# Kernel tuning notes

Measured on AMD Instinct MI355X. Metric: run time of the kernel, lower is better.

The kernel has to match this reference:

```python
import jax, jax.numpy as jnp
import numpy as np

V, E, H, W, S, T, B = 10000, 256, 512, 256, 512, 128, 64


def setup_inputs() -> dict:
    key = jax.random.key(0)
    ks = jax.random.split(key, 17)
    def rn(k, shape, s=0.08):
        return jax.random.normal(k, shape, jnp.float32) * s
    return {
        "tokens": jax.random.randint(ks[0], (B, S), 0, V),
        "dec_h0": jax.random.normal(ks[1], (B, H), jnp.float32),
        "emb_table": rn(ks[2], (V, E), 1.0),
        "enc_Wih": rn(ks[3], (4 * H, E)),
        "enc_Whh": rn(ks[4], (4 * H, H)),
        "enc_bih": rn(ks[5], (4 * H,)),
        "enc_bhh": rn(ks[6], (4 * H,)),
        "dec_Wih": rn(ks[7], (4 * H, E)),
        "dec_Whh": rn(ks[8], (4 * H, H)),
        "dec_bih": rn(ks[9], (4 * H,)),
        "dec_bhh": rn(ks[10], (4 * H,)),
        "W1_w": rn(ks[11], (W, H)),
        "W1_b": rn(ks[12], (W,)),
        "W2_w": rn(ks[13], (W, H)),
        "W2_b": rn(ks[14], (W,)),
        "vt_w": rn(ks[15], (1, W)),
        "vt_b": rn(ks[16], (1,)),
    }


def _lstm_cell(x, h, c, Wih, Whh, bih, bhh):
    # PyTorch gate order: input, forget, cell(g), output
    gates = x @ Wih.T + h @ Whh.T + bih + bhh
    i, f, g, o = jnp.split(gates, 4, axis=-1)
    c = jax.nn.sigmoid(f) * c + jax.nn.sigmoid(i) * jnp.tanh(g)
    h = jax.nn.sigmoid(o) * jnp.tanh(c)
    return h, c


def reference(tokens, dec_h0, emb_table, enc_Wih, enc_Whh, enc_bih, enc_bhh,
              dec_Wih, dec_Whh, dec_bih, dec_bhh, W1_w, W1_b, W2_w, W2_b,
              vt_w, vt_b):
    emb = emb_table[tokens]                       # [B,S,E]
    x_sbe = jnp.swapaxes(emb, 0, 1)               # [S,B,E] time-major
    bsz = tokens.shape[0]
    h0 = jnp.zeros((bsz, enc_Whh.shape[1]), emb.dtype)

    def enc_step(carry, x):
        h, c = carry
        h, c = _lstm_cell(x, h, c, enc_Wih, enc_Whh, enc_bih, enc_bhh)
        return (h, c), h

    _, enc_states = jax.lax.scan(enc_step, (h0, h0), x_sbe)   # [S,B,H]

    # W1(encoder_states) is constant across decoder steps -> hoist it
    blend1 = enc_states @ W1_w.T + W1_b            # [S,B,W]
    c0 = enc_states[-1]                            # original uses last enc state as cell init
    dec_in = jnp.zeros((bsz, emb_table.shape[1]), emb.dtype)  # never updated in original

    def dec_step(carry, _):
        h, c = carry
        h, c = _lstm_cell(dec_in, h, c, dec_Wih, dec_Whh, dec_bih, dec_bhh)
        blend2 = h @ W2_w.T + W2_b                 # [B,W]
        u = (jnp.tanh(blend1 + blend2[None]) @ vt_w.T)[..., 0] + vt_b[0]  # [S,B]
        logp = jax.nn.log_softmax(u.T, axis=1)     # [B,S], softmax over seq positions
        return (h, c), logp

    _, probs = jax.lax.scan(dec_step, (dec_h0, c0), None, length=T)  # [T,B,S]
    return jnp.swapaxes(probs, 0, 1)               # [B,T,S]
```

## Files before the change

### kernel.cpp

```cpp
#include <hip/hip_runtime.h>
#include <hip/hip_bf16.h>
#include <cstdint>
#include <cstddef>

typedef __bf16 bf16_t;
typedef __bf16 bf16x8 __attribute__((ext_vector_type(8)));
typedef float  f32x4  __attribute__((ext_vector_type(4)));

#define NB 64
#define NS 512
#define NTD 128
#define NE 256
#define NH 512
#define NG 2048
#define NW 256

#define HSTEP_DW 16384u

__device__ __forceinline__ float sigm_f(float x) { return 1.f / (1.f + __expf(-x)); }
__device__ __forceinline__ float tanh_f(float x) {
  float e = __expf(2.f * x);
  return 1.f - 2.f / (e + 1.f);
}
__device__ __forceinline__ float bits2f(uint32_t b16) {
  uint32_t u = b16 << 16;
  return __builtin_bit_cast(float, u);
}
__device__ __forceinline__ uint32_t packh(float a, float b) {
  uint16_t lo = __builtin_bit_cast(uint16_t, (bf16_t)a);
  uint16_t hi = __builtin_bit_cast(uint16_t, (bf16_t)b);
  return (uint32_t)lo | ((uint32_t)hi << 16);
}
__device__ __forceinline__ uint32_t aload(const uint32_t* p) {
  return __hip_atomic_load(p, __ATOMIC_RELAXED, __HIP_MEMORY_SCOPE_AGENT);
}
__device__ __forceinline__ uint64_t aload64(const uint64_t* p) {
  return __hip_atomic_load(p, __ATOMIC_RELAXED, __HIP_MEMORY_SCOPE_AGENT);
}
__device__ __forceinline__ void astore(uint32_t* p, uint32_t v) {
  __hip_atomic_store(p, v, __ATOMIC_RELAXED, __HIP_MEMORY_SCOPE_AGENT);
}
__device__ __forceinline__ void astoref(float* p, float v) {
  __hip_atomic_store((uint32_t*)p, __builtin_bit_cast(uint32_t, v),
                     __ATOMIC_RELAXED, __HIP_MEMORY_SCOPE_AGENT);
}
__device__ __forceinline__ float aloadf(const float* p) {
  return __builtin_bit_cast(float, aload((const uint32_t*)p));
}

__global__ __launch_bounds__(256) void pack_b(const float* __restrict__ src,
                                              bf16_t* __restrict__ dst,
                                              int N, int K) {
  int idx = blockIdx.x * 256 + threadIdx.x;
  if (idx >= N * K) return;
  int n = idx / K, k = idx - n * K;
  int lane = (((k & 31) >> 3) << 4) | (n & 15);
  size_t o = ((((size_t)(n >> 4) * (K >> 5)) + (k >> 5)) * 64 + lane) * 8 + (k & 7);
  dst[o] = (bf16_t)src[idx];
}

__global__ __launch_bounds__(256) void gather_emb(const int* __restrict__ tokens,
                                                  const float* __restrict__ table,
                                                  bf16_t* __restrict__ embfrag) {
  int idx = blockIdx.x * 256 + threadIdx.x;
  int row = idx >> 5, e0 = (idx & 31) << 3;
  int b = row & 63, s = row >> 6;
  int tok = tokens[b * NS + s];
  const float4* p = (const float4*)(table + (size_t)tok * NE + e0);
  float4 v0 = p[0], v1 = p[1];
  bf16x8 v;
  v[0] = (bf16_t)v0.x; v[1] = (bf16_t)v0.y; v[2] = (bf16_t)v0.z; v[3] = (bf16_t)v0.w;
  v[4] = (bf16_t)v1.x; v[5] = (bf16_t)v1.y; v[6] = (bf16_t)v1.z; v[7] = (bf16_t)v1.w;
  int mt = row >> 4;
  int ks = e0 >> 5;
  int lane = (b & 15) | (((e0 >> 3) & 3) << 4);
  *(bf16x8*)(embfrag + ((size_t)(mt * 8 + ks) * 64 + lane) * 8) = v;
}

__global__ __launch_bounds__(256) void pack_h0(const float* __restrict__ src,
                                               uint32_t* __restrict__ dst) {
  int idx = blockIdx.x * 256 + threadIdx.x;
  int b = idx >> 8, jp = idx & 255;
  int j = jp * 2;
  float lo = src[(size_t)b * NH + j], hi = src[(size_t)b * NH + j + 1];
  int bg = b >> 4, bl = b & 15, ks = j >> 5;
  int lane = bl | (((j >> 3) & 3) << 4);
  dst[((size_t)bg * 16 + ks) * 256 + lane * 4 + ((j >> 1) & 3)] = packh(lo, hi);
}

template <typename OutT, int KS, int MT>
__global__ __launch_bounds__(256) void gemm_fa2(const bf16_t* __restrict__ A,
                                                const bf16_t* __restrict__ Bp,
                                                OutT* __restrict__ out,
                                                const float* __restrict__ bias1,
                                                const float* __restrict__ bias2,
                                                int N) {
  int lane = threadIdx.x & 63, w = threadIdx.x >> 6;
  int nt = blockIdx.x * 4 + w;
  int mt0 = blockIdx.y * MT;
  bf16x8 bfr[KS];
  const bf16_t* bp = Bp + ((size_t)nt * KS * 64 + lane) * 8;
#pragma unroll
  for (int ks = 0; ks < KS; ++ks) bfr[ks] = *(const bf16x8*)(bp + (size_t)ks * 512);
  int col = (nt << 4) + (lane & 15);
  float bs = bias1[col] + (bias2 ? bias2[col] : 0.f);
  for (int m = 0; m < MT; ++m) {
    int mt = mt0 + m;
    const bf16_t* ap = A + (size_t)mt * (KS * 512) + lane * 8;
    f32x4 acc = {0.f, 0.f, 0.f, 0.f};
#pragma unroll
    for (int ks = 0; ks < KS; ++ks)
      acc = __builtin_amdgcn_mfma_f32_16x16x32_bf16(
          *(const bf16x8*)(ap + (size_t)ks * 512), bfr[ks], acc, 0, 0, 0);
    int rbase = (mt << 4) + ((lane >> 4) << 2);
#pragma unroll
    for (int r = 0; r < 4; ++r)
      out[(size_t)(rbase + r) * N + col] = (OutT)(acc[r] + bs);
  }
}

__global__ __launch_bounds__(256) void enc_chain(
    const bf16_t* __restrict__ Wp, const bf16_t* __restrict__ xih,
    const bf16_t* __restrict__ W1p, const float* __restrict__ W1_b,
    uint32_t* __restrict__ hfrag, uint32_t* __restrict__ flags,
    bf16_t* __restrict__ blend1) {
  __shared__ bf16_t wlds[8 * 8192];
  __shared__ bf16_t w1lds[8192];
  __shared__ float gl[4][16][36];
  const int T = NS;
  int tid = threadIdx.x, lane = tid & 63, wv = tid >> 6;
  int bg = blockIdx.x >> 4, slice = blockIdx.x & 15;

  for (int l = 0; l < 8; ++l) {
    int g = l >> 1, p = l & 1;
    const bf16_t* src = Wp + (size_t)(g * 32 + slice * 2 + p) * 8192;
    bf16_t* dst = wlds + (size_t)l * 8192;
    for (int i = tid; i < 1024; i += 256)
      *(bf16x8*)(dst + (size_t)i * 8) = *(const bf16x8*)(src + (size_t)i * 8);
  }
  {
    const bf16_t* src = W1p + (size_t)slice * 8192;
    for (int i = tid; i < 1024; i += 256)
      *(bf16x8*)(w1lds + (size_t)i * 8) = *(const bf16x8*)(src + (size_t)i * 8);
  }

  int ub = tid >> 4, uj2 = tid & 15;
  int lane_f = ub | ((uj2 >> 2) << 4);
  float c0 = 0.f, c1 = 0.f;
  float b1bias = W1_b[slice * 16 + (lane & 15)];
  __syncthreads();

  const uint64_t* hq = (const uint64_t*)hfrag;
  uint32_t* fl = flags + bg * 16;

  for (int t = 0; t <= T; ++t) {
    uint32_t xd[4];
    if (t < T) {
      const uint32_t* xr = (const uint32_t*)xih +
          ((size_t)(t * 64 + bg * 16 + ub)) * 1024 + slice * 16 + uj2;
#pragma unroll
      for (int g = 0; g < 4; ++g) xd[g] = xr[(size_t)g * 256];
    }
    if (t > 0) {
      if (wv == 0) {
        uint32_t tgt = (uint32_t)t;
        bool ok;
        do {
          uint32_t f = tgt;
          if (lane < 16 && lane != (uint32_t)slice) f = aload(fl + lane);
          ok = __all(f >= tgt);
        } while (!ok);
      }
      __syncthreads();
    }
    const uint64_t* hb = hq + ((size_t)t * 4 + bg) * 2048 + lane * 2;
    uint64_t aq[16][2];
#pragma unroll
    for (int ks = 0; ks < 16; ++ks) {
      aq[ks][0] = aload64(hb + (size_t)ks * 128);
      aq[ks][1] = aload64(hb + (size_t)ks * 128 + 1);
    }
    if (t >= 1 && wv == 0) {
      f32x4 bacc = {0.f, 0.f, 0.f, 0.f};
#pragma unroll
      for (int ks = 0; ks < 16; ++ks) {
        union { uint64_t q[2]; bf16x8 v; } u;
        u.q[0] = aq[ks][0]; u.q[1] = aq[ks][1];
        bacc = __builtin_amdgcn_mfma_f32_16x16x32_bf16(
            u.v, *(const bf16x8*)(w1lds + (size_t)ks * 512 + lane * 8), bacc, 0, 0, 0);
      }
      int col = slice * 16 + (lane & 15);
      int rb = (lane >> 4) << 2;
      size_t rowb = (size_t)(t - 1) * 64 + bg * 16 + rb;
#pragma unroll
      for (int r = 0; r < 4; ++r)
        blend1[(rowb + r) * 256 + col] = (bf16_t)(bacc[r] + b1bias);
    }
    if (t < T) {
      const bf16_t* wl = wlds + (size_t)(wv * 2) * 8192 + lane * 8;
      f32x4 acc0 = {0.f, 0.f, 0.f, 0.f}, acc1 = {0.f, 0.f, 0.f, 0.f};
#pragma unroll
      for (int ks = 0; ks < 16; ++ks) {
        union { uint64_t q[2]; bf16x8 v; } u;
        u.q[0] = aq[ks][0]; u.q[1] = aq[ks][1];
        acc0 = __builtin_amdgcn_mfma_f32_16x16x32_bf16(
            u.v, *(const bf16x8*)(wl + (size_t)ks * 512), acc0, 0, 0, 0);
        acc1 = __builtin_amdgcn_mfma_f32_16x16x32_bf16(
            u.v, *(const bf16x8*)(wl + 8192 + (size_t)ks * 512), acc1, 0, 0, 0);
      }
      int cc = lane & 15, rb = (lane >> 4) << 2;
#pragma unroll
      for (int r = 0; r < 4; ++r) {
        gl[wv][rb + r][cc] = acc0[r];
        gl[wv][rb + r][16 + cc] = acc1[r];
      }
      __syncthreads();
      float p[4][2];
#pragma unroll
      for (int g = 0; g < 4; ++g) {
        p[g][0] = gl[g][ub][uj2 * 2] + bits2f(xd[g] & 0xffffu);
        p[g][1] = gl[g][ub][uj2 * 2 + 1] + bits2f(xd[g] >> 16);
      }
      float i0 = sigm_f(p[0][0]), f0 = sigm_f(p[1][0]);
      float g0 = tanh_f(p[2][0]), o0 = sigm_f(p[3][0]);
      c0 = f0 * c0 + i0 * g0;
      float h0 = o0 * tanh_f(c0);
      float i1 = sigm_f(p[0][1]), f1 = sigm_f(p[1][1]);
      float g1 = tanh_f(p[2][1]), o1 = sigm_f(p[3][1]);
      c1 = f1 * c1 + i1 * g1;
      float h1 = o1 * tanh_f(c1);
      astore(hfrag + ((size_t)(t + 1) * 4 + bg) * 4096 +
                 slice * 256 + lane_f * 4 + (uj2 & 3), packh(h0, h1));
      __syncthreads();
      if (tid == 0) astore(fl + slice, (uint32_t)(t + 1));
    }
  }
}

__global__ __launch_bounds__(256) void dec_attn(
    const bf16_t* __restrict__ Wp, const float* __restrict__ bih,
    const float* __restrict__ bhh, const bf16_t* __restrict__ W2p,
    const float* __restrict__ W2_b, uint32_t* __restrict__ hfrag,
    const uint32_t* __restrict__ c0frag, uint32_t* __restrict__ hflags,
    uint32_t* __restrict__ bl2f, const bf16_t* __restrict__ blend1,
    float* __restrict__ blend2, const float* __restrict__ vt_w,
    float* __restrict__ out) {
  union SM {
    struct { bf16_t wlds[8 * 8192]; bf16_t w2lds[8192]; float gl[4][16][36]; } c;
    struct { float vt[272], b2[272], u[512], red[8]; } a;
  };
  __shared__ SM sm;
  const int T = NTD;
  int tid = threadIdx.x, lane = tid & 63, wv = tid >> 6;

  if (blockIdx.x < 64) {
    int bg = blockIdx.x >> 4, slice = blockIdx.x & 15;
    for (int l = 0; l < 8; ++l) {
      int g = l >> 1, p = l & 1;
      const bf16_t* src = Wp + (size_t)(g * 32 + slice * 2 + p) * 8192;
      bf16_t* dst = sm.c.wlds + (size_t)l * 8192;
      for (int i = tid; i < 1024; i += 256)
        *(bf16x8*)(dst + (size_t)i * 8) = *(const bf16x8*)(src + (size_t)i * 8);
    }
    {
      const bf16_t* src = W2p + (size_t)slice * 8192;
      for (int i = tid; i < 1024; i += 256)
        *(bf16x8*)(sm.c.w2lds + (size_t)i * 8) = *(const bf16x8*)(src + (size_t)i * 8);
    }
    int ub = tid >> 4, uj2 = tid & 15;
    int j_lo = slice * 32 + uj2 * 2;
    int lane_f = ub | ((uj2 >> 2) << 4);
    uint32_t d = c0frag[((size_t)bg * 16 + slice) * 256 + lane_f * 4 + (uj2 & 3)];
    float c0 = bits2f(d & 0xffffu), c1 = bits2f(d >> 16);
    float bsum[4][2];
#pragma unroll
    for (int g = 0; g < 4; ++g) {
      bsum[g][0] = bih[g * NH + j_lo] + bhh[g * NH + j_lo];
      bsum[g][1] = bih[g * NH + j_lo + 1] + bhh[g * NH + j_lo + 1];
    }
    float b2bias = W2_b[slice * 16 + (lane & 15)];
    __syncthreads();

    const uint64_t* hq = (const uint64_t*)hfrag;
    uint32_t* fl = hflags + bg * 16;

    for (int t = 0; t <= T; ++t) {
      if (t > 0) {
        if (wv == 0) {
          uint32_t tgt = (uint32_t)t;
          bool ok;
          do {
            uint32_t f = tgt;
            if (lane < 16 && lane != (uint32_t)slice) f = aload(fl + lane);
            ok = __all(f >= tgt);
          } while (!ok);
        }
        __syncthreads();
      }
      const uint64_t* hb = hq + ((size_t)t * 4 + bg) * 2048 + lane * 2;
      uint64_t aq[16][2];
#pragma unroll
      for (int ks = 0; ks < 16; ++ks) {
        aq[ks][0] = aload64(hb + (size_t)ks * 128);
        aq[ks][1] = aload64(hb + (size_t)ks * 128 + 1);
      }
      if (t >= 1 && wv == 0) {
        f32x4 bacc = {0.f, 0.f, 0.f, 0.f};
#pragma unroll
        for (int ks = 0; ks < 16; ++ks) {
          union { uint64_t q[2]; bf16x8 v; } u;
          u.q[0] = aq[ks][0]; u.q[1] = aq[ks][1];
          bacc = __builtin_amdgcn_mfma_f32_16x16x32_bf16(
              u.v, *(const bf16x8*)(sm.c.w2lds + (size_t)ks * 512 + lane * 8),
              bacc, 0, 0, 0);
        }
        int col = slice * 16 + (lane & 15);
        int rb = (lane >> 4) << 2;
        size_t rowb = (size_t)(t - 1) * 64 + bg * 16 + rb;
#pragma unroll
        for (int r = 0; r < 4; ++r)
          astoref(blend2 + (rowb + r) * 256 + col, bacc[r] + b2bias);
      }
      if (t < T) {
        const bf16_t* wl = sm.c.wlds + (size_t)(wv * 2) * 8192 + lane * 8;
        f32x4 acc0 = {0.f, 0.f, 0.f, 0.f}, acc1 = {0.f, 0.f, 0.f, 0.f};
#pragma unroll
        for (int ks = 0; ks < 16; ++ks) {
          union { uint64_t q[2]; bf16x8 v; } u;
          u.q[0] = aq[ks][0]; u.q[1] = aq[ks][1];
          acc0 = __builtin_amdgcn_mfma_f32_16x16x32_bf16(
              u.v, *(const bf16x8*)(wl + (size_t)ks * 512), acc0, 0, 0, 0);
          acc1 = __builtin_amdgcn_mfma_f32_16x16x32_bf16(
              u.v, *(const bf16x8*)(wl + 8192 + (size_t)ks * 512), acc1, 0, 0, 0);
        }
        int cc = lane & 15, rb = (lane >> 4) << 2;
#pragma unroll
        for (int r = 0; r < 4; ++r) {
          sm.c.gl[wv][rb + r][cc] = acc0[r];
          sm.c.gl[wv][rb + r][16 + cc] = acc1[r];
        }
        __syncthreads();
        float p[4][2];
#pragma unroll
        for (int g = 0; g < 4; ++g) {
          p[g][0] = sm.c.gl[g][ub][uj2 * 2] + bsum[g][0];
          p[g][1] = sm.c.gl[g][ub][uj2 * 2 + 1] + bsum[g][1];
        }
        float i0 = sigm_f(p[0][0]), f0 = sigm_f(p[1][0]);
        float g0 = tanh_f(p[2][0]), o0 = sigm_f(p[3][0]);
        c0 = f0 * c0 + i0 * g0;
        float h0 = o0 * tanh_f(c0);
        float i1 = sigm_f(p[0][1]), f1 = sigm_f(p[1][1]);
        float g1 = tanh_f(p[2][1]), o1 = sigm_f(p[3][1]);
        c1 = f1 * c1 + i1 * g1;
        float h1 = o1 * tanh_f(c1);
        astore(hfrag + ((size_t)(t + 1) * 4 + bg) * 4096 +
                   slice * 256 + lane_f * 4 + (uj2 & 3), packh(h0, h1));
        __syncthreads();
        if (tid == 0) {
          astore(fl + slice, (uint32_t)(t + 1));
          astore(bl2f + bg * 16 + slice, (uint32_t)t);
        }
      } else {
        __syncthreads();
        if (tid == 0) astore(bl2f + bg * 16 + slice, (uint32_t)T);
      }
    }
  } else {
    int w = blockIdx.x - 64;
    for (int k = w; k < NTD * NB; k += 192) {
      int t = k >> 6, b = k & 63;
      if (wv == 0) {
        uint32_t tgt = (uint32_t)(t + 1);
        bool ok;
        do {
          uint32_t f = aload(bl2f + lane);
          ok = __all(f >= tgt);
          if (!ok) __builtin_amdgcn_s_sleep(16);
        } while (!ok);
      }
      __syncthreads();
      {
        int ww = tid;
        int pi = ww + ((ww >> 6) << 2);
        sm.a.vt[pi] = vt_w[ww];
        sm.a.b2[pi] = aloadf(blend2 + (size_t)(t * 64 + b) * NW + ww);
      }
      __syncthreads();
      int wgrp = lane >> 4, sgrp = lane & 15;
      int base = wgrp * 68;
      for (int it = 0; it < 8; ++it) {
        int s = it * 64 + wv * 16 + sgrp;
        const bf16_t* row = blend1 + ((size_t)s * NB + b) * NW + wgrp * 64;
        float val = 0.f;
#pragma unroll
        for (int c8 = 0; c8 < 8; ++c8) {
          bf16x8 v = *(const bf16x8*)(row + c8 * 8);
#pragma unroll
          for (int jx = 0; jx < 8; ++jx) {
            int wi = base + c8 * 8 + jx;
            val += sm.a.vt[wi] * tanh_f((float)v[jx] + sm.a.b2[wi]);
          }
        }
        val += __shfl_xor(val, 16, 64);
        val += __shfl_xor(val, 32, 64);
        if (wgrp == 0) sm.a.u[it * 64 + wv * 16 + sgrp] = val;
      }
      __syncthreads();
      float a = sm.a.u[tid], bb2 = sm.a.u[tid + 256];
      float m = fmaxf(a, bb2);
#pragma unroll
      for (int o = 1; o < 64; o <<= 1) m = fmaxf(m, __shfl_xor(m, o, 64));
      if (lane == 0) sm.a.red[wv] = m;
      __syncthreads();
      m = fmaxf(fmaxf(sm.a.red[0], sm.a.red[1]), fmaxf(sm.a.red[2], sm.a.red[3]));
      float e = __expf(a - m) + __expf(bb2 - m);
#pragma unroll
      for (int o = 1; o < 64; o <<= 1) e += __shfl_xor(e, o, 64);
      if (lane == 0) sm.a.red[4 + wv] = e;
      __syncthreads();
      float lz = m + logf(sm.a.red[4] + sm.a.red[5] + sm.a.red[6] + sm.a.red[7]);
      size_t ob = ((size_t)b * NTD + t) * NS;
      out[ob + tid] = a - lz;
      out[ob + tid + 256] = bb2 - lz;
      __syncthreads();
    }
  }
}

extern "C" void kernel_launch(void* const* d_in, const int* in_sizes, int n_in,
                              void* d_out, int out_size, void* d_ws, size_t ws_size,
                              hipStream_t stream) {
  const int*   tokens    = (const int*)d_in[0];
  const float* dec_h0    = (const float*)d_in[1];
  const float* emb_table = (const float*)d_in[2];
  const float* enc_Wih   = (const float*)d_in[3];
  const float* enc_Whh   = (const float*)d_in[4];
  const float* enc_bih   = (const float*)d_in[5];
  const float* enc_bhh   = (const float*)d_in[6];
  const float* dec_Whh   = (const float*)d_in[8];
  const float* dec_bih   = (const float*)d_in[9];
  const float* dec_bhh   = (const float*)d_in[10];
  const float* W1_w      = (const float*)d_in[11];
  const float* W1_b      = (const float*)d_in[12];
  const float* W2_w      = (const float*)d_in[13];
  const float* W2_b      = (const float*)d_in[14];
  const float* vt_w      = (const float*)d_in[15];
  float* out = (float*)d_out;

  char* w = (char*)d_ws;
  size_t off = 0;
  auto alloc = [&](size_t bytes) {
    size_t o = off;
    off += (bytes + 255) & ~(size_t)255;
    return o;
  };
  bf16_t* embfrag = (bf16_t*)(w + alloc((size_t)NS * NB * NE * 2));
  bf16_t* xih     = (bf16_t*)(w + alloc((size_t)NS * NB * NG * 2));
  uint32_t* enc_hf = (uint32_t*)(w + alloc((size_t)(NS + 1) * HSTEP_DW * 4));
  uint32_t* dec_hf = (uint32_t*)(w + alloc((size_t)(NTD + 1) * HSTEP_DW * 4));
  bf16_t* blend1  = (bf16_t*)(w + alloc((size_t)NS * NB * NW * 2));
  float*  blend2  = (float*)(w + alloc((size_t)NTD * NB * NW * 4));
  bf16_t* pWih    = (bf16_t*)(w + alloc((size_t)NG * NE * 2));
  bf16_t* pWhhE   = (bf16_t*)(w + alloc((size_t)NG * NH * 2));
  bf16_t* pWhhD   = (bf16_t*)(w + alloc((size_t)NG * NH * 2));
  bf16_t* pW1     = (bf16_t*)(w + alloc((size_t)NW * NH * 2));
  bf16_t* pW2     = (bf16_t*)(w + alloc((size_t)NW * NH * 2));
  uint32_t* flags = (uint32_t*)(w + alloc(1024));
  (void)ws_size; (void)in_sizes; (void)n_in; (void)out_size;

  hipMemsetAsync(flags, 0, 768, stream);
  hipMemsetAsync(enc_hf, 0, HSTEP_DW * 4, stream);

  pack_b<<<(NG * NE) / 256, 256, 0, stream>>>(enc_Wih, pWih, NG, NE);
  pack_b<<<(NG * NH) / 256, 256, 0, stream>>>(enc_Whh, pWhhE, NG, NH);
  pack_b<<<(NG * NH) / 256, 256, 0, stream>>>(dec_Whh, pWhhD, NG, NH);
  pack_b<<<(NW * NH) / 256, 256, 0, stream>>>(W1_w, pW1, NW, NH);
  pack_b<<<(NW * NH) / 256, 256, 0, stream>>>(W2_w, pW2, NW, NH);

  gather_emb<<<(NS * NB * (NE / 8)) / 256, 256, 0, stream>>>(tokens, emb_table, embfrag);
  pack_h0<<<64, 256, 0, stream>>>(dec_h0, dec_hf);

  gemm_fa2<bf16_t, 8, 16><<<dim3(128 / 4, 2048 / 16), 256, 0, stream>>>(
      embfrag, pWih, xih, enc_bih, enc_bhh, NG);

  enc_chain<<<64, 256, 0, stream>>>(pWhhE, xih, pW1, W1_b, enc_hf, flags, blend1);

  dec_attn<<<256, 256, 0, stream>>>(pWhhD, dec_bih, dec_bhh, pW2, W2_b, dec_hf,
                                    enc_hf + (size_t)NS * HSTEP_DW, flags + 64,
                                    flags + 128, blend1, blend2, vt_w, out);
}
```

Measured before the change: 3.243 ms.

## Restructure LSTM recurrence waves to drop block barriers and use per-wave flags

The recurrent encoder and decoder blocks are reorganized so each of two waves computes all four gates for a 16-column tile directly in registers. This removes the LDS gate exchange and the block-wide __syncthreads in every timestep. A third wave independently computes the W1/W2 projection by polling per-wave padded flags, and the fourth wave exits. The input-projection GEMM now writes xih in a fragment layout matched to the new per-wave gate ownership. The cost is more flags to poll (32 per group) and an explicit vmcnt drain before each flag publish.

```diff
diff --git a/kernel.cpp b/kernel.cpp
--- a/kernel.cpp
+++ b/kernel.cpp
@@ -16,6 +16,7 @@
 #define NW 256
 
 #define HSTEP_DW 16384u
+#define FPAD 16
 
 __device__ __forceinline__ float sigm_f(float x) { return 1.f / (1.f + __expf(-x)); }
 __device__ __forceinline__ float tanh_f(float x) {
@@ -26,11 +27,6 @@
   uint32_t u = b16 << 16;
   return __builtin_bit_cast(float, u);
 }
-__device__ __forceinline__ uint32_t packh(float a, float b) {
-  uint16_t lo = __builtin_bit_cast(uint16_t, (bf16_t)a);
-  uint16_t hi = __builtin_bit_cast(uint16_t, (bf16_t)b);
-  return (uint32_t)lo | ((uint32_t)hi << 16);
-}
 __device__ __forceinline__ uint32_t aload(const uint32_t* p) {
   return __hip_atomic_load(p, __ATOMIC_RELAXED, __HIP_MEMORY_SCOPE_AGENT);
 }
@@ -46,6 +42,13 @@
 }
 __device__ __forceinline__ float aloadf(const float* p) {
   return __builtin_bit_cast(float, aload((const uint32_t*)p));
+}
+__device__ __forceinline__ void drain_vm() {
+  asm volatile("s_waitcnt vmcnt(0)" ::: "memory");
+}
+__device__ __forceinline__ float xpick(uint2 v, int r) {
+  uint32_t d = (r < 2) ? v.x : v.y;
+  return bits2f((r & 1) ? (d >> 16) : (d & 0xffffu));
 }
 
 __global__ __launch_bounds__(256) void pack_b(const float* __restrict__ src,
@@ -83,18 +86,20 @@
   int b = idx >> 8, jp = idx & 255;
   int j = jp * 2;
   float lo = src[(size_t)b * NH + j], hi = src[(size_t)b * NH + j + 1];
+  uint16_t l16 = __builtin_bit_cast(uint16_t, (bf16_t)lo);
+  uint16_t h16 = __builtin_bit_cast(uint16_t, (bf16_t)hi);
   int bg = b >> 4, bl = b & 15, ks = j >> 5;
   int lane = bl | (((j >> 3) & 3) << 4);
-  dst[((size_t)bg * 16 + ks) * 256 + lane * 4 + ((j >> 1) & 3)] = packh(lo, hi);
-}
-
-template <typename OutT, int KS, int MT>
-__global__ __launch_bounds__(256) void gemm_fa2(const bf16_t* __restrict__ A,
+  dst[((size_t)bg * 16 + ks) * 256 + lane * 4 + ((j >> 1) & 3)] =
+      (uint32_t)l16 | ((uint32_t)h16 << 16);
+}
+
+__global__ __launch_bounds__(256) void gemm_xih(const bf16_t* __restrict__ A,
                                                 const bf16_t* __restrict__ Bp,
-                                                OutT* __restrict__ out,
-                                                const float* __restrict__ bias1,
-                                                const float* __restrict__ bias2,
-                                                int N) {
+                                                bf16_t* __restrict__ out,
+                                                const float* __restrict__ b1,
+                                                const float* __restrict__ b2) {
+  const int KS = 8, MT = 16;
   int lane = threadIdx.x & 63, w = threadIdx.x >> 6;
   int nt = blockIdx.x * 4 + w;
   int mt0 = blockIdx.y * MT;
@@ -102,8 +107,9 @@
   const bf16_t* bp = Bp + ((size_t)nt * KS * 64 + lane) * 8;
 #pragma unroll
   for (int ks = 0; ks < KS; ++ks) bfr[ks] = *(const bf16x8*)(bp + (size_t)ks * 512);
-  int col = (nt << 4) + (lane & 15);
-  float bs = bias1[col] + (bias2 ? bias2[col] : 0.f);
+  int n = (nt << 4) + (lane & 15);
+  float bs = b1[n] + b2[n];
+  int g = nt >> 5, sl = (nt & 31) >> 1, ct = nt & 1;
   for (int m = 0; m < MT; ++m) {
     int mt = mt0 + m;
     const bf16_t* ap = A + (size_t)mt * (KS * 512) + lane * 8;
@@ -112,127 +118,127 @@
     for (int ks = 0; ks < KS; ++ks)
       acc = __builtin_amdgcn_mfma_f32_16x16x32_bf16(
           *(const bf16x8*)(ap + (size_t)ks * 512), bfr[ks], acc, 0, 0, 0);
-    int rbase = (mt << 4) + ((lane >> 4) << 2);
-#pragma unroll
-    for (int r = 0; r < 4; ++r)
-      out[(size_t)(rbase + r) * N + col] = (OutT)(acc[r] + bs);
+    ushort4 hv;
+    hv.x = __builtin_bit_cast(uint16_t, (bf16_t)(acc[0] + bs));
+    hv.y = __builtin_bit_cast(uint16_t, (bf16_t)(acc[1] + bs));
+    hv.z = __builtin_bit_cast(uint16_t, (bf16_t)(acc[2] + bs));
+    hv.w = __builtin_bit_cast(uint16_t, (bf16_t)(acc[3] + bs));
+    *(ushort4*)(out + ((((size_t)mt * 16 + sl) * 2 + ct) * 4 + g) * 256 + lane * 4) = hv;
   }
 }
 
 __global__ __launch_bounds__(256) void enc_chain(
-    const bf16_t* __restrict__ Wp, const bf16_t* __restrict__ xih,
+    const bf16_t* __restrict__ Wp, const bf16_t* __restrict__ xih2,
     const bf16_t* __restrict__ W1p, const float* __restrict__ W1_b,
     uint32_t* __restrict__ hfrag, uint32_t* __restrict__ flags,
     bf16_t* __restrict__ blend1) {
   __shared__ bf16_t wlds[8 * 8192];
-  __shared__ bf16_t w1lds[8192];
-  __shared__ float gl[4][16][36];
-  const int T = NS;
-  int tid = threadIdx.x, lane = tid & 63, wv = tid >> 6;
+  __shared__ bf16_t wb[8192];
+  int tid = threadIdx.x, lane = tid & 63, wid = tid >> 6;
   int bg = blockIdx.x >> 4, slice = blockIdx.x & 15;
 
   for (int l = 0; l < 8; ++l) {
     int g = l >> 1, p = l & 1;
-    const bf16_t* src = Wp + (size_t)(g * 32 + slice * 2 + p) * 8192;
-    bf16_t* dst = wlds + (size_t)l * 8192;
+    const bf16_t* s = Wp + (size_t)(g * 32 + slice * 2 + p) * 8192;
     for (int i = tid; i < 1024; i += 256)
-      *(bf16x8*)(dst + (size_t)i * 8) = *(const bf16x8*)(src + (size_t)i * 8);
+      *(bf16x8*)(wlds + l * 8192 + (size_t)i * 8) = *(const bf16x8*)(s + (size_t)i * 8);
   }
   {
-    const bf16_t* src = W1p + (size_t)slice * 8192;
+    const bf16_t* s = W1p + (size_t)slice * 8192;
     for (int i = tid; i < 1024; i += 256)
-      *(bf16x8*)(w1lds + (size_t)i * 8) = *(const bf16x8*)(src + (size_t)i * 8);
+      *(bf16x8*)(wb + (size_t)i * 8) = *(const bf16x8*)(s + (size_t)i * 8);
   }
-
-  int ub = tid >> 4, uj2 = tid & 15;
-  int lane_f = ub | ((uj2 >> 2) << 4);
-  float c0 = 0.f, c1 = 0.f;
-  float b1bias = W1_b[slice * 16 + (lane & 15)];
   __syncthreads();
+  if (wid == 3) return;
 
   const uint64_t* hq = (const uint64_t*)hfrag;
-  uint32_t* fl = flags + bg * 16;
-
-  for (int t = 0; t <= T; ++t) {
-    uint32_t xd[4];
-    if (t < T) {
-      const uint32_t* xr = (const uint32_t*)xih +
-          ((size_t)(t * 64 + bg * 16 + ub)) * 1024 + slice * 16 + uj2;
-#pragma unroll
-      for (int g = 0; g < 4; ++g) xd[g] = xr[(size_t)g * 256];
-    }
-    if (t > 0) {
-      if (wv == 0) {
-        uint32_t tgt = (uint32_t)t;
-        bool ok;
+  uint32_t* fbase = flags + bg * 32 * FPAD;
+  int c = lane & 15, grp = lane >> 4;
+
+  if (wid < 2) {
+    int ct = wid;
+    int j = slice * 32 + ct * 16 + c;
+    int sub = (j >> 3) & 3, dw = (j >> 1) & 3;
+    uint32_t* myflag = fbase + (slice * 2 + ct) * FPAD;
+    float cst[4] = {0.f, 0.f, 0.f, 0.f};
+    const bf16_t* wb0 = wlds + (size_t)(0 * 2 + ct) * 8192;
+    const bf16_t* wb1 = wlds + (size_t)(1 * 2 + ct) * 8192;
+    const bf16_t* wb2 = wlds + (size_t)(2 * 2 + ct) * 8192;
+    const bf16_t* wb3 = wlds + (size_t)(3 * 2 + ct) * 8192;
+    for (int t = 0; t < NS; ++t) {
+      const uint32_t* xb = (const uint32_t*)xih2 +
+          ((((size_t)t * 4 + bg) * 16 + slice) * 2 + ct) * 512 + lane * 2;
+      uint2 xg0 = *(const uint2*)(xb);
+      uint2 xg1 = *(const uint2*)(xb + 128);
+      uint2 xg2 = *(const uint2*)(xb + 256);
+      uint2 xg3 = *(const uint2*)(xb + 384);
+      if (t > 0) {
+        uint32_t tgt = (uint32_t)t; bool ok;
         do {
           uint32_t f = tgt;
-          if (lane < 16 && lane != (uint32_t)slice) f = aload(fl + lane);
+          if (lane < 32) f = aload(fbase + lane * FPAD);
           ok = __all(f >= tgt);
         } while (!ok);
       }
-      __syncthreads();
-    }
-    const uint64_t* hb = hq + ((size_t)t * 4 + bg) * 2048 + lane * 2;
-    uint64_t aq[16][2];
-#pragma unroll
-    for (int ks = 0; ks < 16; ++ks) {
-      aq[ks][0] = aload64(hb + (size_t)ks * 128);
-      aq[ks][1] = aload64(hb + (size_t)ks * 128 + 1);
-    }
-    if (t >= 1 && wv == 0) {
-      f32x4 bacc = {0.f, 0.f, 0.f, 0.f};
+      const uint64_t* hb = hq + ((size_t)t * 4 + bg) * 2048 + lane * 2;
+      uint64_t aq[16][2];
+#pragma unroll
+      for (int ks = 0; ks < 16; ++ks) {
+        aq[ks][0] = aload64(hb + (size_t)ks * 128);
+        aq[ks][1] = aload64(hb + (size_t)ks * 128 + 1);
+      }
+      f32x4 a0 = {0.f,0.f,0.f,0.f}, a1 = a0, a2 = a0, a3 = a0;
 #pragma unroll
       for (int ks = 0; ks < 16; ++ks) {
         union { uint64_t q[2]; bf16x8 v; } u;
         u.q[0] = aq[ks][0]; u.q[1] = aq[ks][1];
-        bacc = __builtin_amdgcn_mfma_f32_16x16x32_bf16(
-            u.v, *(const bf16x8*)(w1lds + (size_t)ks * 512 + lane * 8), bacc, 0, 0, 0);
-      }
-      int col = slice * 16 + (lane & 15);
-      int rb = (lane >> 4) << 2;
-      size_t rowb = (size_t)(t - 1) * 64 + bg * 16 + rb;
-#pragma unroll
-      for (int r = 0; r < 4; ++r)
-        blend1[(rowb + r) * 256 + col] = (bf16_t)(bacc[r] + b1bias);
-    }
-    if (t < T) {
-      const bf16_t* wl = wlds + (size_t)(wv * 2) * 8192 + lane * 8;
-      f32x4 acc0 = {0.f, 0.f, 0.f, 0.f}, acc1 = {0.f, 0.f, 0.f, 0.f};
+        int o = ks * 512 + lane * 8;
+        a0 = __builtin_amdgcn_mfma_f32_16x16x32_bf16(u.v, *(const bf16x8*)(wb0 + o), a0, 0, 0, 0);
+        a1 = __builtin_amdgcn_mfma_f32_16x16x32_bf16(u.v, *(const bf16x8*)(wb1 + o), a1, 0, 0, 0);
+        a2 = __builtin_amdgcn_mfma_f32_16x16x32_bf16(u.v, *(const bf16x8*)(wb2 + o), a2, 0, 0, 0);
+        a3 = __builtin_amdgcn_mfma_f32_16x16x32_bf16(u.v, *(const bf16x8*)(wb3 + o), a3, 0, 0, 0);
+      }
+      uint32_t hsb = ((uint32_t)(t + 1) * 4 + (uint32_t)bg) * 4096 + slice * 256;
+#pragma unroll
+      for (int r = 0; r < 4; ++r) {
+        float pi = a0[r] + xpick(xg0, r), pf = a1[r] + xpick(xg1, r);
+        float pg = a2[r] + xpick(xg2, r), po = a3[r] + xpick(xg3, r);
+        float iG = sigm_f(pi), fG = sigm_f(pf), gG = tanh_f(pg), oG = sigm_f(po);
+        cst[r] = fG * cst[r] + iG * gG;
+        float h = oG * tanh_f(cst[r]);
+        uint16_t hv = __builtin_bit_cast(uint16_t, (bf16_t)h);
+        uint32_t other = (uint32_t)__shfl_xor((int)(uint32_t)hv, 1, 64);
+        if (!(lane & 1)) {
+          uint32_t dword = (uint32_t)hv | (other << 16);
+          astore(hfrag + (size_t)hsb + (((grp * 4 + r) | (sub << 4)) * 4 + dw), dword);
+        }
+      }
+      drain_vm();
+      if (lane == 0) astore(myflag, (uint32_t)(t + 1));
+    }
+  } else {
+    float bb = W1_b[slice * 16 + c];
+    for (int t = 1; t <= NS; ++t) {
+      uint32_t tgt = (uint32_t)t; bool ok;
+      do {
+        uint32_t f = tgt;
+        if (lane < 32) f = aload(fbase + lane * FPAD);
+        ok = __all(f >= tgt);
+      } while (!ok);
+      const uint64_t* hb = hq + ((size_t)t * 4 + bg) * 2048 + lane * 2;
+      f32x4 acc = {0.f, 0.f, 0.f, 0.f};
 #pragma unroll
       for (int ks = 0; ks < 16; ++ks) {
         union { uint64_t q[2]; bf16x8 v; } u;
-        u.q[0] = aq[ks][0]; u.q[1] = aq[ks][1];
-        acc0 = __builtin_amdgcn_mfma_f32_16x16x32_bf16(
-            u.v, *(const bf16x8*)(wl + (size_t)ks * 512), acc0, 0, 0, 0);
-        acc1 = __builtin_amdgcn_mfma_f32_16x16x32_bf16(
-            u.v, *(const bf16x8*)(wl + 8192 + (size_t)ks * 512), acc1, 0, 0, 0);
-      }
-      int cc = lane & 15, rb = (lane >> 4) << 2;
-#pragma unroll
-      for (int r = 0; r < 4; ++r) {
-        gl[wv][rb + r][cc] = acc0[r];
-        gl[wv][rb + r][16 + cc] = acc1[r];
-      }
-      __syncthreads();
-      float p[4][2];
-#pragma unroll
-      for (int g = 0; g < 4; ++g) {
-        p[g][0] = gl[g][ub][uj2 * 2] + bits2f(xd[g] & 0xffffu);
-        p[g][1] = gl[g][ub][uj2 * 2 + 1] + bits2f(xd[g] >> 16);
-      }
-      float i0 = sigm_f(p[0][0]), f0 = sigm_f(p[1][0]);
-      float g0 = tanh_f(p[2][0]), o0 = sigm_f(p[3][0]);
-      c0 = f0 * c0 + i0 * g0;
-      float h0 = o0 * tanh_f(c0);
-      float i1 = sigm_f(p[0][1]), f1 = sigm_f(p[1][1]);
-      float g1 = tanh_f(p[2][1]), o1 = sigm_f(p[3][1]);
-      c1 = f1 * c1 + i1 * g1;
-      float h1 = o1 * tanh_f(c1);
-      astore(hfrag + ((size_t)(t + 1) * 4 + bg) * 4096 +
-                 slice * 256 + lane_f * 4 + (uj2 & 3), packh(h0, h1));
-      __syncthreads();
-      if (tid == 0) astore(fl + slice, (uint32_t)(t + 1));
+        u.q[0] = aload64(hb + (size_t)ks * 128);
+        u.q[1] = aload64(hb + (size_t)ks * 128 + 1);
+        acc = __builtin_amdgcn_mfma_f32_16x16x32_bf16(
+            u.v, *(const bf16x8*)(wb + ks * 512 + lane * 8), acc, 0, 0, 0);
+      }
+      size_t row = (size_t)(t - 1) * 64 + bg * 16 + grp * 4;
+#pragma unroll
+      for (int r = 0; r < 4; ++r)
+        blend1[(row + r) * 256 + slice * 16 + c] = (bf16_t)(acc[r] + bb);
     }
   }
 }
@@ -241,140 +247,139 @@
     const bf16_t* __restrict__ Wp, const float* __restrict__ bih,
     const float* __restrict__ bhh, const bf16_t* __restrict__ W2p,
     const float* __restrict__ W2_b, uint32_t* __restrict__ hfrag,
-    const uint32_t* __restrict__ c0frag, uint32_t* __restrict__ hflags,
+    const uint32_t* __restrict__ c0frag, uint32_t* __restrict__ dflags,
     uint32_t* __restrict__ bl2f, const bf16_t* __restrict__ blend1,
     float* __restrict__ blend2, const float* __restrict__ vt_w,
     float* __restrict__ out) {
   union SM {
-    struct { bf16_t wlds[8 * 8192]; bf16_t w2lds[8192]; float gl[4][16][36]; } c;
+    struct { bf16_t wlds[8 * 8192]; bf16_t wb[8192]; } c;
     struct { float vt[272], b2[272], u[512], red[8]; } a;
   };
   __shared__ SM sm;
-  const int T = NTD;
-  int tid = threadIdx.x, lane = tid & 63, wv = tid >> 6;
+  int tid = threadIdx.x, lane = tid & 63, wid = tid >> 6;
 
   if (blockIdx.x < 64) {
     int bg = blockIdx.x >> 4, slice = blockIdx.x & 15;
     for (int l = 0; l < 8; ++l) {
       int g = l >> 1, p = l & 1;
-      const bf16_t* src = Wp + (size_t)(g * 32 + slice * 2 + p) * 8192;
-      bf16_t* dst = sm.c.wlds + (size_t)l * 8192;
+      const bf16_t* s = Wp + (size_t)(g * 32 + slice * 2 + p) * 8192;
       for (int i = tid; i < 1024; i += 256)
-        *(bf16x8*)(dst + (size_t)i * 8) = *(const bf16x8*)(src + (size_t)i * 8);
+        *(bf16x8*)(sm.c.wlds + l * 8192 + (size_t)i * 8) = *(const bf16x8*)(s + (size_t)i * 8);
     }
     {
-      const bf16_t* src = W2p + (size_t)slice * 8192;
+      const bf16_t* s = W2p + (size_t)slice * 8192;
       for (int i = tid; i < 1024; i += 256)
-        *(bf16x8*)(sm.c.w2lds + (size_t)i * 8) = *(const bf16x8*)(src + (size_t)i * 8);
-    }
-    int ub = tid >> 4, uj2 = tid & 15;
-    int j_lo = slice * 32 + uj2 * 2;
-    int lane_f = ub | ((uj2 >> 2) << 4);
-    uint32_t d = c0frag[((size_t)bg * 16 + slice) * 256 + lane_f * 4 + (uj2 & 3)];
-    float c0 = bits2f(d & 0xffffu), c1 = bits2f(d >> 16);
-    float bsum[4][2];
-#pragma unroll
-    for (int g = 0; g < 4; ++g) {
-      bsum[g][0] = bih[g * NH + j_lo] + bhh[g * NH + j_lo];
-      bsum[g][1] = bih[g * NH + j_lo + 1] + bhh[g * NH + j_lo + 1];
-    }
-    float b2bias = W2_b[slice * 16 + (lane & 15)];
+        *(bf16x8*)(sm.c.wb + (size_t)i * 8) = *(const bf16x8*)(s + (size_t)i * 8);
+    }
     __syncthreads();
+    if (wid == 3) return;
 
     const uint64_t* hq = (const uint64_t*)hfrag;
-    uint32_t* fl = hflags + bg * 16;
-
-    for (int t = 0; t <= T; ++t) {
-      if (t > 0) {
-        if (wv == 0) {
-          uint32_t tgt = (uint32_t)t;
-          bool ok;
+    uint32_t* fbase = dflags + bg * 32 * FPAD;
+    int c = lane & 15, grp = lane >> 6 ? 0 : lane >> 4;
+    grp = lane >> 4;
+
+    if (wid < 2) {
+      int ct = wid;
+      int j = slice * 32 + ct * 16 + c;
+      int sub = (j >> 3) & 3, dw = (j >> 1) & 3, half = j & 1;
+      uint32_t* myflag = fbase + (slice * 2 + ct) * FPAD;
+      float bs0 = bih[0 * NH + j] + bhh[0 * NH + j];
+      float bs1 = bih[1 * NH + j] + bhh[1 * NH + j];
+      float bs2 = bih[2 * NH + j] + bhh[2 * NH + j];
+      float bs3 = bih[3 * NH + j] + bhh[3 * NH + j];
+      float cst[4];
+#pragma unroll
+      for (int r = 0; r < 4; ++r) {
+        uint32_t d = c0frag[(size_t)(bg * 16 + slice) * 256 +
+                            (((grp * 4 + r) | (sub << 4)) * 4 + dw)];
+        cst[r] = half ? bits2f(d >> 16) : bits2f(d & 0xffffu);
+      }
+      const bf16_t* wb0 = sm.c.wlds + (size_t)(0 * 2 + ct) * 8192;
+      const bf16_t* wb1 = sm.c.wlds + (size_t)(1 * 2 + ct) * 8192;
+      const bf16_t* wb2 = sm.c.wlds + (size_t)(2 * 2 + ct) * 8192;
+      const bf16_t* wb3 = sm.c.wlds + (size_t)(3 * 2 + ct) * 8192;
+      for (int t = 0; t < NTD; ++t) {
+        if (t > 0) {
+          uint32_t tgt = (uint32_t)t; bool ok;
           do {
             uint32_t f = tgt;
-            if (lane < 16 && lane != (uint32_t)slice) f = aload(fl + lane);
+            if (lane < 32) f = aload(fbase + lane * FPAD);
             ok = __all(f >= tgt);
           } while (!ok);
         }
-        __syncthreads();
-      }
-      const uint64_t* hb = hq + ((size_t)t * 4 + bg) * 2048 + lane * 2;
-      uint64_t aq[16][2];
-#pragma unroll
-      for (int ks = 0; ks < 16; ++ks) {
-        aq[ks][0] = aload64(hb + (size_t)ks * 128);
-        aq[ks][1] = aload64(hb + (size_t)ks * 128 + 1);
-      }
-      if (t >= 1 && wv == 0) {
-        f32x4 bacc = {0.f, 0.f, 0.f, 0.f};
+        const uint64_t* hb = hq + ((size_t)t * 4 + bg) * 2048 + lane * 2;
+        uint64_t aq[16][2];
+#pragma unroll
+        for (int ks = 0; ks < 16; ++ks) {
+          aq[ks][0] = aload64(hb + (size_t)ks * 128);
+          aq[ks][1] = aload64(hb + (size_t)ks * 128 + 1);
+        }
+        f32x4 a0 = {0.f,0.f,0.f,0.f}, a1 = a0, a2 = a0, a3 = a0;
 #pragma unroll
         for (int ks = 0; ks < 16; ++ks) {
           union { uint64_t q[2]; bf16x8 v; } u;
           u.q[0] = aq[ks][0]; u.q[1] = aq[ks][1];
-          bacc = __builtin_amdgcn_mfma_f32_16x16x32_bf16(
-              u.v, *(const bf16x8*)(sm.c.w2lds + (size_t)ks * 512 + lane * 8),
-              bacc, 0, 0, 0);
-        }
-        int col = slice * 16 + (lane & 15);
-        int rb = (lane >> 4) << 2;
-        size_t rowb = (size_t)(t - 1) * 64 + bg * 16 + rb;
-#pragma unroll
-        for (int r = 0; r < 4; ++r)
-          astoref(blend2 + (rowb + r) * 256 + col, bacc[r] + b2bias);
-      }
-      if (t < T) {
-        const bf16_t* wl = sm.c.wlds + (size_t)(wv * 2) * 8192 + lane * 8;
-        f32x4 acc0 = {0.f, 0.f, 0.f, 0.f}, acc1 = {0.f, 0.f, 0.f, 0.f};
+          int o = ks * 512 + lane * 8;
+          a0 = __builtin_amdgcn_mfma_f32_16x16x32_bf16(u.v, *(const bf16x8*)(wb0 + o), a0, 0, 0, 0);
+          a1 = __builtin_amdgcn_mfma_f32_16x16x32_bf16(u.v, *(const bf16x8*)(wb1 + o), a1, 0, 0, 0);
+          a2 = __builtin_amdgcn_mfma_f32_16x16x32_bf16(u.v, *(const bf16x8*)(wb2 + o), a2, 0, 0, 0);
+          a3 = __builtin_amdgcn_mfma_f32_16x16x32_bf16(u.v, *(const bf16x8*)(wb3 + o), a3, 0, 0, 0);
+        }
+        uint32_t hsb = ((uint32_t)(t + 1) * 4 + (uint32_t)bg) * 4096 + slice * 256;
+#pragma unroll
+        for (int r = 0; r < 4; ++r) {
+          float iG = sigm_f(a0[r] + bs0), fG = sigm_f(a1[r] + bs1);
+          float gG = tanh_f(a2[r] + bs2), oG = sigm_f(a3[r] + bs3);
+          cst[r] = fG * cst[r] + iG * gG;
+          float h = oG * tanh_f(cst[r]);
+          uint16_t hv = __builtin_bit_cast(uint16_t, (bf16_t)h);
+          uint32_t other = (uint32_t)__shfl_xor((int)(uint32_t)hv, 1, 64);
+          if (!(lane & 1)) {
+            uint32_t dword = (uint32_t)hv | (other << 16);
+            astore(hfrag + (size_t)hsb + (((grp * 4 + r) | (sub << 4)) * 4 + dw), dword);
+          }
+        }
+        drain_vm();
+        if (lane == 0) astore(myflag, (uint32_t)(t + 1));
+      }
+    } else {
+      float bb = W2_b[slice * 16 + c];
+      uint32_t* myb = bl2f + (bg * 16 + slice) * FPAD;
+      for (int t = 1; t <= NTD; ++t) {
+        uint32_t tgt = (uint32_t)t; bool ok;
+        do {
+          uint32_t f = tgt;
+          if (lane < 32) f = aload(fbase + lane * FPAD);
+          ok = __all(f >= tgt);
+        } while (!ok);
+        const uint64_t* hb = hq + ((size_t)t * 4 + bg) * 2048 + lane * 2;
+        f32x4 acc = {0.f, 0.f, 0.f, 0.f};
 #pragma unroll
         for (int ks = 0; ks < 16; ++ks) {
           union { uint64_t q[2]; bf16x8 v; } u;
-          u.q[0] = aq[ks][0]; u.q[1] = aq[ks][1];
-          acc0 = __builtin_amdgcn_mfma_f32_16x16x32_bf16(
-              u.v, *(const bf16x8*)(wl + (size_t)ks * 512), acc0, 0, 0, 0);
-          acc1 = __builtin_amdgcn_mfma_f32_16x16x32_bf16(
-              u.v, *(const bf16x8*)(wl + 8192 + (size_t)ks * 512), acc1, 0, 0, 0);
-        }
-        int cc = lane & 15, rb = (lane >> 4) << 2;
-#pragma unroll
-        for (int r = 0; r < 4; ++r) {
-          sm.c.gl[wv][rb + r][cc] = acc0[r];
-          sm.c.gl[wv][rb + r][16 + cc] = acc1[r];
-        }
-        __syncthreads();
-        float p[4][2];
-#pragma unroll
-        for (int g = 0; g < 4; ++g) {
-          p[g][0] = sm.c.gl[g][ub][uj2 * 2] + bsum[g][0];
-          p[g][1] = sm.c.gl[g][ub][uj2 * 2 + 1] + bsum[g][1];
-        }
-        float i0 = sigm_f(p[0][0]), f0 = sigm_f(p[1][0]);
-        float g0 = tanh_f(p[2][0]), o0 = sigm_f(p[3][0]);
-        c0 = f0 * c0 + i0 * g0;
-        float h0 = o0 * tanh_f(c0);
-        float i1 = sigm_f(p[0][1]), f1 = sigm_f(p[1][1]);
-        float g1 = tanh_f(p[2][1]), o1 = sigm_f(p[3][1]);
-        c1 = f1 * c1 + i1 * g1;
-        float h1 = o1 * tanh_f(c1);
-        astore(hfrag + ((size_t)(t + 1) * 4 + bg) * 4096 +
-                   slice * 256 + lane_f * 4 + (uj2 & 3), packh(h0, h1));
-        __syncthreads();
-        if (tid == 0) {
-          astore(fl + slice, (uint32_t)(t + 1));
-          astore(bl2f + bg * 16 + slice, (uint32_t)t);
-        }
-      } else {
-        __syncthreads();
-        if (tid == 0) astore(bl2f + bg * 16 + slice, (uint32_t)T);
+          u.q[0] = aload64(hb + (size_t)ks * 128);
+          u.q[1] = aload64(hb + (size_t)ks * 128 + 1);
+          acc = __builtin_amdgcn_mfma_f32_16x16x32_bf16(
+              u.v, *(const bf16x8*)(sm.c.wb + ks * 512 + lane * 8), acc, 0, 0, 0);
+        }
+        size_t row = (size_t)(t - 1) * 64 + bg * 16 + grp * 4;
+#pragma unroll
+        for (int r = 0; r < 4; ++r)
+          astoref(blend2 + (row + r) * 256 + slice * 16 + c, acc[r] + bb);
+        drain_vm();
+        if (lane == 0) astore(myb, (uint32_t)t);
       }
     }
   } else {
     int w = blockIdx.x - 64;
     for (int k = w; k < NTD * NB; k += 192) {
-      int t = k >> 6, b = k & 63;
-      if (wv == 0) {
-        uint32_t tgt = (uint32_t)(t + 1);
-        bool ok;
+      int t = k >> 6, b = k & 63, bgb = b >> 4;
+      if (wid == 0) {
+        uint32_t tgt = (uint32_t)(t + 1); bool ok;
         do {
-          uint32_t f = aload(bl2f + lane);
+          uint32_t f = tgt;
+          if (lane < 16) f = aload(bl2f + (bgb * 16 + lane) * FPAD);
           ok = __all(f >= tgt);
           if (!ok) __builtin_amdgcn_s_sleep(16);
         } while (!ok);
@@ -390,7 +395,7 @@
       int wgrp = lane >> 4, sgrp = lane & 15;
       int base = wgrp * 68;
       for (int it = 0; it < 8; ++it) {
-        int s = it * 64 + wv * 16 + sgrp;
+        int s = it * 64 + wid * 16 + sgrp;
         const bf16_t* row = blend1 + ((size_t)s * NB + b) * NW + wgrp * 64;
         float val = 0.f;
 #pragma unroll
@@ -404,20 +409,20 @@
         }
         val += __shfl_xor(val, 16, 64);
         val += __shfl_xor(val, 32, 64);
-        if (wgrp == 0) sm.a.u[it * 64 + wv * 16 + sgrp] = val;
+        if (wgrp == 0) sm.a.u[it * 64 + wid * 16 + sgrp] = val;
       }
       __syncthreads();
       float a = sm.a.u[tid], bb2 = sm.a.u[tid + 256];
       float m = fmaxf(a, bb2);
 #pragma unroll
       for (int o = 1; o < 64; o <<= 1) m = fmaxf(m, __shfl_xor(m, o, 64));
-      if (lane == 0) sm.a.red[wv] = m;
+      if (lane == 0) sm.a.red[wid] = m;
       __syncthreads();
       m = fmaxf(fmaxf(sm.a.red[0], sm.a.red[1]), fmaxf(sm.a.red[2], sm.a.red[3]));
       float e = __expf(a - m) + __expf(bb2 - m);
 #pragma unroll
       for (int o = 1; o < 64; o <<= 1) e += __shfl_xor(e, o, 64);
-      if (lane == 0) sm.a.red[4 + wv] = e;
+      if (lane == 0) sm.a.red[4 + wid] = e;
       __syncthreads();
       float lz = m + logf(sm.a.red[4] + sm.a.red[5] + sm.a.red[6] + sm.a.red[7]);
       size_t ob = ((size_t)b * NTD + t) * NS;
@@ -456,7 +461,7 @@
     return o;
   };
   bf16_t* embfrag = (bf16_t*)(w + alloc((size_t)NS * NB * NE * 2));
-  bf16_t* xih     = (bf16_t*)(w + alloc((size_t)NS * NB * NG * 2));
+  bf16_t* xih2    = (bf16_t*)(w + alloc((size_t)NS * NB * NG * 2));
   uint32_t* enc_hf = (uint32_t*)(w + alloc((size_t)(NS + 1) * HSTEP_DW * 4));
   uint32_t* dec_hf = (uint32_t*)(w + alloc((size_t)(NTD + 1) * HSTEP_DW * 4));
   bf16_t* blend1  = (bf16_t*)(w + alloc((size_t)NS * NB * NW * 2));
@@ -466,10 +471,10 @@
   bf16_t* pWhhD   = (bf16_t*)(w + alloc((size_t)NG * NH * 2));
   bf16_t* pW1     = (bf16_t*)(w + alloc((size_t)NW * NH * 2));
   bf16_t* pW2     = (bf16_t*)(w + alloc((size_t)NW * NH * 2));
-  uint32_t* flags = (uint32_t*)(w + alloc(1024));
+  uint32_t* flags = (uint32_t*)(w + alloc(5120 * 4));
   (void)ws_size; (void)in_sizes; (void)n_in; (void)out_size;
 
-  hipMemsetAsync(flags, 0, 768, stream);
+  hipMemsetAsync(flags, 0, 5120 * 4, stream);
   hipMemsetAsync(enc_hf, 0, HSTEP_DW * 4, stream);
 
   pack_b<<<(NG * NE) / 256, 256, 0, stream>>>(enc_Wih, pWih, NG, NE);
@@ -481,12 +486,13 @@
   gather_emb<<<(NS * NB * (NE / 8)) / 256, 256, 0, stream>>>(tokens, emb_table, embfrag);
   pack_h0<<<64, 256, 0, stream>>>(dec_h0, dec_hf);
 
-  gemm_fa2<bf16_t, 8, 16><<<dim3(128 / 4, 2048 / 16), 256, 0, stream>>>(
-      embfrag, pWih, xih, enc_bih, enc_bhh, NG);
-
-  enc_chain<<<64, 256, 0, stream>>>(pWhhE, xih, pW1, W1_b, enc_hf, flags, blend1);
+  gemm_xih<<<dim3(128 / 4, 2048 / 16), 256, 0, stream>>>(
+      embfrag, pWih, xih2, enc_bih, enc_bhh);
+
+  enc_chain<<<64, 256, 0, stream>>>(pWhhE, xih2, pW1, W1_b, enc_hf, flags, blend1);
 
   dec_attn<<<256, 256, 0, stream>>>(pWhhD, dec_bih, dec_bhh, pW2, W2_b, dec_hf,
-                                    enc_hf + (size_t)NS * HSTEP_DW, flags + 64,
-                                    flags + 128, blend1, blend2, vt_w, out);
-}
+                                    enc_hf + (size_t)NS * HSTEP_DW,
+                                    flags + 2048, flags + 4096,
+                                    blend1, blend2, vt_w, out);
+}
```

Result: no change. 3.285 ms (+1.3%).
